# Performance work log

Hardware: AMD Instinct MI355X
Metric: run time of the kernel (lower is better)

## Reference

```python
import jax, jax.numpy as jnp
import numpy as np

B, N, H, D = 1024, 128, 128, 8  # batch, num_nodes (= num variables), hidden, diffusion size


def setup_inputs() -> dict:
    key = jax.random.key(0)
    ks = jax.random.split(key, 7)
    return {
        "x": jax.random.normal(ks[0], (B, N), dtype=jnp.float32),
        "f_weight": jax.random.normal(ks[1], (N, N, H), dtype=jnp.float32) * 0.1,
        "g_weight": jax.random.normal(ks[2], (N, N, H, D), dtype=jnp.float32) * 0.1,
        "Wf": jax.random.normal(ks[3], (N, H), dtype=jnp.float32) * (1.0 / np.sqrt(H)),
        "bf": jax.random.normal(ks[4], (N,), dtype=jnp.float32) * 0.01,
        "Wg": jax.random.normal(ks[5], (N, H), dtype=jnp.float32) * (1.0 / np.sqrt(H)),
        "bg": jax.random.normal(ks[6], (N,), dtype=jnp.float32) * 0.01,
    }


def reference(x, f_weight, g_weight, Wf, bf, Wg, bg):
    # Drift f: per node i, temp_i = x @ f_weight[i]  -> [B,H]; out_i = fc_i(elu(temp_i)) -> [B,1]
    # Batched over nodes as a single einsum instead of the original Python loop.
    temp_f = jnp.einsum('bn,inh->bih', x, f_weight)              # [B,N,H]
    f_out = jnp.einsum('bih,ih->bi', jax.nn.elu(temp_f), Wf) + bf  # [B,N]

    # Diffusion g: per node i, temp_i = x @ g_weight[i] -> [B,H,D]; fc_i applied over H per diffusion channel.
    temp_g = jnp.einsum('bn,inhd->bihd', x, g_weight)            # [B,N,H,D]
    g_out = jnp.einsum('bihd,ih->bid', jax.nn.elu(temp_g), Wg) + bg[None, :, None]  # [B,N,D]
    return f_out, g_out
```

## Files before the change

kernel.cpp:

```cpp
#include <hip/hip_runtime.h>
#include <hip/hip_bf16.h>


typedef unsigned short u16;
typedef __attribute__((ext_vector_type(8))) short bf16x8;
typedef __attribute__((ext_vector_type(4))) float f32x4;

typedef __attribute__((address_space(1))) const void* gas_ptr;
typedef __attribute__((address_space(3))) void* las_ptr;
#define GLOAD_LDS16(g, l) __builtin_amdgcn_global_load_lds((gas_ptr)(g), (las_ptr)(l), 16, 0, 0)

#define WS_W_ELEMS  ((size_t)128 * 1152 * 128)
#define WS_X_ELEMS  ((size_t)1024 * 128)
#define WS_NEED_BYTES ((WS_W_ELEMS + WS_X_ELEMS) * 2)

__device__ __forceinline__ u16 f2bf(float f) {
    unsigned int u = __float_as_uint(f);
    u += 0x7fffu + ((u >> 16) & 1u);
    return (u16)(u >> 16);
}
__device__ __forceinline__ uint32_t pack2bf(float a, float b) {
    return (uint32_t)f2bf(a) | ((uint32_t)f2bf(b) << 16);
}
__device__ __forceinline__ float elu(float v) {
    return v > 0.f ? v : __expf(v) - 1.f;
}

__global__ void sde_prepass_w(const float* __restrict__ fw, const float* __restrict__ gw,
                              u16* __restrict__ wsW) {
    __shared__ u16 tile[128 * 130];
    const int t   = threadIdx.x;
    const int blk = blockIdx.x;
    const int i   = blk / 9;
    const int ct  = blk % 9;
    const float* src;
    int sstride;
    if (ct < 8) { src = gw + (size_t)i * 131072 + ct * 128; sstride = 1024; }
    else        { src = fw + (size_t)i * 16384;             sstride = 128;  }
    const int c4 = (t & 31) * 4;
    const int np = (t >> 5) * 2;
    for (int p = 0; p < 8; ++p) {
        int n = p * 16 + np;
        float4 v0 = *(const float4*)&src[(size_t)n * sstride + c4];
        float4 v1 = *(const float4*)&src[(size_t)(n + 1) * sstride + c4];
        *(uint32_t*)&tile[(c4 + 0) * 130 + n] = pack2bf(v0.x, v1.x);
        *(uint32_t*)&tile[(c4 + 1) * 130 + n] = pack2bf(v0.y, v1.y);
        *(uint32_t*)&tile[(c4 + 2) * 130 + n] = pack2bf(v0.z, v1.z);
        *(uint32_t*)&tile[(c4 + 3) * 130 + n] = pack2bf(v0.w, v1.w);
    }
    __syncthreads();
    const int n0 = (t & 63) * 2;
    uint32_t* dst32 = (uint32_t*)wsW;
    for (int p = 0; p < 32; ++p) {
        int c = p * 4 + (t >> 6);
        uint32_t v = *(const uint32_t*)&tile[c * 130 + n0];
        dst32[((size_t)i * 1152 + ct * 128 + c) * 64 + (t & 63)] = v;
    }
}

__global__ void sde_prepass_x(const float* __restrict__ x, u16* __restrict__ wsX) {
    const int tid = blockIdx.x * 256 + threadIdx.x;
    float4 v = ((const float4*)x)[tid];
    ((uint2*)wsX)[tid] = make_uint2(pack2bf(v.x, v.y), pack2bf(v.z, v.w));
}

__global__ __launch_bounds__(256) void sde_mfma(
    const u16* __restrict__ wsAll,
    const float* __restrict__ Wf, const float* __restrict__ bfp,
    const float* __restrict__ Wg, const float* __restrict__ bgp,
    float* __restrict__ out)
{
    __shared__ u16 xs[128 * 128];
    __shared__ u16 wst[64 * 128];
    __shared__ float wgs[128];
    __shared__ float wfs[128];

    const int t    = threadIdx.x;
    const int bx   = blockIdx.x;
    const int i    = bx & 127;
    const int b0   = (bx >> 7) << 7;
    const int w    = t >> 6;
    const int lane = t & 63;
    const int l15  = lane & 15;
    const int quad = lane >> 4;
    const int rl   = lane >> 4;
    const int j16  = lane & 15;
    const int sw   = l15 & 7;

    const u16* wsW = wsAll;
    const u16* wsX = wsAll + WS_W_ELEMS;

    if (t < 128) { wgs[t] = Wg[i * 128 + t]; wfs[t] = Wf[i * 128 + t]; }

    {
        const char* srcX = (const char*)(wsX + (size_t)b0 * 128);
        #pragma unroll
        for (int r = 0; r < 8; ++r) {
            int row = w * 32 + r * 4 + rl;
            int soff = row * 256 + ((j16 ^ (row & 7)) << 4);
            GLOAD_LDS16(srcX + soff, (char*)xs + w * 8192 + r * 1024);
        }
    }

    float racc[8], frac[8];
    #pragma unroll
    for (int q = 0; q < 8; ++q) { racc[q] = 0.f; frac[q] = 0.f; }

    for (int ct = 0; ct < 18; ++ct) {
        {
            const char* srcW = (const char*)(wsW + ((size_t)i * 1152 + ct * 64) * 128);
            #pragma unroll
            for (int r = 0; r < 4; ++r) {
                int row = w * 16 + r * 4 + rl;
                int soff = row * 256 + ((j16 ^ (row & 7)) << 4);
                GLOAD_LDS16(srcW + soff, (char*)wst + w * 4096 + r * 1024);
            }
        }
        __syncthreads();

        f32x4 acc[2][4];
        #pragma unroll
        for (int rs = 0; rs < 2; ++rs)
            #pragma unroll
            for (int cs = 0; cs < 4; ++cs)
                acc[rs][cs] = (f32x4){0.f, 0.f, 0.f, 0.f};

        const int r0 = w * 32 + l15;
        #pragma unroll
        for (int kk = 0; kk < 4; ++kk) {
            const int co = ((kk * 4 + quad) ^ sw) << 3;
            bf16x8 a0 = *(const bf16x8*)&xs[r0 * 128 + co];
            bf16x8 a1 = *(const bf16x8*)&xs[(r0 + 16) * 128 + co];
            bf16x8 bv[4];
            #pragma unroll
            for (int cs = 0; cs < 4; ++cs)
                bv[cs] = *(const bf16x8*)&wst[(cs * 16 + l15) * 128 + co];
            #pragma unroll
            for (int cs = 0; cs < 4; ++cs) {
                acc[0][cs] = __builtin_amdgcn_mfma_f32_16x16x32_bf16(a0, bv[cs], acc[0][cs], 0, 0, 0);
                acc[1][cs] = __builtin_amdgcn_mfma_f32_16x16x32_bf16(a1, bv[cs], acc[1][cs], 0, 0, 0);
            }
        }

        if (ct < 16) {
            float wv[4];
            #pragma unroll
            for (int cs = 0; cs < 4; ++cs) wv[cs] = wgs[ct * 8 + cs * 2 + (l15 >> 3)];
            #pragma unroll
            for (int rs = 0; rs < 2; ++rs)
                #pragma unroll
                for (int rg = 0; rg < 4; ++rg) {
                    float p = elu(acc[rs][0][rg]) * wv[0] + elu(acc[rs][1][rg]) * wv[1]
                            + elu(acc[rs][2][rg]) * wv[2] + elu(acc[rs][3][rg]) * wv[3];
                    p += __shfl_xor(p, 8);
                    racc[rs * 4 + rg] += p;
                }
        } else {
            float wv[4];
            #pragma unroll
            for (int cs = 0; cs < 4; ++cs) wv[cs] = wfs[(ct - 16) * 64 + cs * 16 + l15];
            #pragma unroll
            for (int rs = 0; rs < 2; ++rs)
                #pragma unroll
                for (int rg = 0; rg < 4; ++rg) {
                    float p = elu(acc[rs][0][rg]) * wv[0] + elu(acc[rs][1][rg]) * wv[1]
                            + elu(acc[rs][2][rg]) * wv[2] + elu(acc[rs][3][rg]) * wv[3];
                    p += __shfl_xor(p, 1);
                    p += __shfl_xor(p, 2);
                    p += __shfl_xor(p, 4);
                    p += __shfl_xor(p, 8);
                    frac[rs * 4 + rg] += p;
                }
        }
        __syncthreads();
    }

    const float bfv = bfp[i], bgv = bgp[i];
    #pragma unroll
    for (int rs = 0; rs < 2; ++rs)
        #pragma unroll
        for (int rg = 0; rg < 4; ++rg) {
            int row = w * 32 + rs * 16 + quad * 4 + rg;
            size_t brow = (size_t)(b0 + row);
            if (l15 == 0)
                out[brow * 128 + i] = frac[rs * 4 + rg] + bfv;
            if (l15 < 8)
                out[(size_t)131072 + (brow * 128 + i) * 8 + (lane & 7)] = racc[rs * 4 + rg] + bgv;
        }
}

__global__ void sde_fallback(const float* __restrict__ x, const float* __restrict__ fw,
                             const float* __restrict__ gw,
                             const float* __restrict__ Wf, const float* __restrict__ bfp,
                             const float* __restrict__ Wg, const float* __restrict__ bgp,
                             float* __restrict__ out)
{
    __shared__ float xsh[64 * 128];
    const int t  = threadIdx.x;
    const int i  = blockIdx.x >> 4;
    const int b0 = (blockIdx.x & 15) << 6;
    for (int idx = t; idx < 64 * 128; idx += 64) xsh[idx] = x[(size_t)b0 * 128 + idx];
    __syncthreads();
    const float* xr  = &xsh[t * 128];
    const float* fwi = fw + (size_t)i * 16384;
    const float* gwi = gw + (size_t)i * 131072;
    float fa = 0.f;
    for (int h = 0; h < 128; ++h) {
        float tf = 0.f;
        for (int n = 0; n < 128; ++n) tf += xr[n] * fwi[n * 128 + h];
        fa += elu(tf) * Wf[i * 128 + h];
    }
    float ga[8];
    #pragma unroll
    for (int d = 0; d < 8; ++d) ga[d] = 0.f;
    for (int h = 0; h < 128; ++h) {
        float tg[8] = {0, 0, 0, 0, 0, 0, 0, 0};
        for (int n = 0; n < 128; ++n) {
            float xv = xr[n];
            const float* gp = gwi + ((size_t)n * 128 + h) * 8;
            #pragma unroll
            for (int d = 0; d < 8; ++d) tg[d] += xv * gp[d];
        }
        float wv = Wg[i * 128 + h];
        #pragma unroll
        for (int d = 0; d < 8; ++d) ga[d] += elu(tg[d]) * wv;
    }
    size_t b = (size_t)(b0 + t);
    out[b * 128 + i] = fa + bfp[i];
    #pragma unroll
    for (int d = 0; d < 8; ++d)
        out[(size_t)131072 + (b * 128 + i) * 8 + d] = ga[d] + bgp[i];
}

extern "C" void kernel_launch(void* const* d_in, const int* in_sizes, int n_in,
                              void* d_out, int out_size, void* d_ws, size_t ws_size,
                              hipStream_t stream) {
    const float* x  = (const float*)d_in[0];
    const float* fw = (const float*)d_in[1];
    const float* gw = (const float*)d_in[2];
    const float* Wf = (const float*)d_in[3];
    const float* bf = (const float*)d_in[4];
    const float* Wg = (const float*)d_in[5];
    const float* bg = (const float*)d_in[6];
    float* out = (float*)d_out;

    if (ws_size >= WS_NEED_BYTES) {
        u16* wsAll = (u16*)d_ws;
        sde_prepass_w<<<1152, 256, 0, stream>>>(fw, gw, wsAll);
        sde_prepass_x<<<128, 256, 0, stream>>>(x, wsAll + WS_W_ELEMS);
        sde_mfma<<<1024, 256, 0, stream>>>(wsAll, Wf, bf, Wg, bg, out);
    } else {
        sde_fallback<<<2048, 64, 0, stream>>>(x, fw, gw, Wf, bf, Wg, bg, out);
    }
}
```

Measured before the change: 185.0 us.

## Keep x fragments in registers, merge prepasses, defer cross-lane reductions

The MFMA kernel now loads its bf16 x A-fragments once from global memory into registers instead of staging a 32 KB x tile in LDS. This cuts LDS use per block and removes the repeated LDS reads of A inside the loop. The kernel adds launch_bounds(256,4) to favour higher occupancy, at the cost of more register pressure. The shuffle reductions that ran every tile are now done once per output at the end. The weight and x bf16 prepasses are merged into one kernel with a direct strided transpose that no longer uses an LDS tile.

```diff
diff --git a/kernel.cpp b/kernel.cpp
--- a/kernel.cpp
+++ b/kernel.cpp
@@ -4,6 +4,7 @@
 
 typedef unsigned short u16;
 typedef __attribute__((ext_vector_type(8))) short bf16x8;
+typedef __attribute__((ext_vector_type(8))) short short8;
 typedef __attribute__((ext_vector_type(4))) float f32x4;
 
 typedef __attribute__((address_space(1))) const void* gas_ptr;
@@ -26,51 +27,48 @@
     return v > 0.f ? v : __expf(v) - 1.f;
 }
 
-__global__ void sde_prepass_w(const float* __restrict__ fw, const float* __restrict__ gw,
-                              u16* __restrict__ wsW) {
-    __shared__ u16 tile[128 * 130];
-    const int t   = threadIdx.x;
-    const int blk = blockIdx.x;
-    const int i   = blk / 9;
-    const int ct  = blk % 9;
-    const float* src;
-    int sstride;
-    if (ct < 8) { src = gw + (size_t)i * 131072 + ct * 128; sstride = 1024; }
-    else        { src = fw + (size_t)i * 16384;             sstride = 128;  }
-    const int c4 = (t & 31) * 4;
-    const int np = (t >> 5) * 2;
-    for (int p = 0; p < 8; ++p) {
-        int n = p * 16 + np;
-        float4 v0 = *(const float4*)&src[(size_t)n * sstride + c4];
-        float4 v1 = *(const float4*)&src[(size_t)(n + 1) * sstride + c4];
-        *(uint32_t*)&tile[(c4 + 0) * 130 + n] = pack2bf(v0.x, v1.x);
-        *(uint32_t*)&tile[(c4 + 1) * 130 + n] = pack2bf(v0.y, v1.y);
-        *(uint32_t*)&tile[(c4 + 2) * 130 + n] = pack2bf(v0.z, v1.z);
-        *(uint32_t*)&tile[(c4 + 3) * 130 + n] = pack2bf(v0.w, v1.w);
-    }
-    __syncthreads();
-    const int n0 = (t & 63) * 2;
-    uint32_t* dst32 = (uint32_t*)wsW;
-    for (int p = 0; p < 32; ++p) {
-        int c = p * 4 + (t >> 6);
-        uint32_t v = *(const uint32_t*)&tile[c * 130 + n0];
-        dst32[((size_t)i * 1152 + ct * 128 + c) * 64 + (t & 63)] = v;
-    }
-}
-
-__global__ void sde_prepass_x(const float* __restrict__ x, u16* __restrict__ wsX) {
-    const int tid = blockIdx.x * 256 + threadIdx.x;
-    float4 v = ((const float4*)x)[tid];
-    ((uint2*)wsX)[tid] = make_uint2(pack2bf(v.x, v.y), pack2bf(v.z, v.w));
-}
-
-__global__ __launch_bounds__(256) void sde_mfma(
+__global__ void sde_prepass(const float* __restrict__ fw, const float* __restrict__ gw,
+                            const float* __restrict__ x, u16* __restrict__ wsW) {
+    const int bx = blockIdx.x;
+    const int t  = threadIdx.x;
+    if (bx < 8192) {
+        const int i  = bx >> 6;
+        const int c  = (((bx >> 4) & 3) << 8) + t;
+        const int n0 = (bx & 15) << 3;
+        const float* src = gw + (size_t)i * 131072;
+        float v[8];
+        #pragma unroll
+        for (int j = 0; j < 8; ++j) v[j] = src[(size_t)(n0 + j) * 1024 + c];
+        short8 o;
+        #pragma unroll
+        for (int j = 0; j < 8; ++j) o[j] = (short)f2bf(v[j]);
+        *(short8*)&wsW[((size_t)i * 1152 + c) * 128 + n0] = o;
+    } else if (bx < 9216) {
+        const int b2 = bx - 8192;
+        const int i  = b2 >> 3;
+        const int c  = t & 127;
+        const int n0 = (((b2 & 7) << 1) + (t >> 7)) << 3;
+        const float* src = fw + (size_t)i * 16384;
+        float v[8];
+        #pragma unroll
+        for (int j = 0; j < 8; ++j) v[j] = src[(size_t)(n0 + j) * 128 + c];
+        short8 o;
+        #pragma unroll
+        for (int j = 0; j < 8; ++j) o[j] = (short)f2bf(v[j]);
+        *(short8*)&wsW[((size_t)i * 1152 + 1024 + c) * 128 + n0] = o;
+    } else {
+        const int tid = (bx - 9216) * 256 + t;
+        float4 v = ((const float4*)x)[tid];
+        ((uint2*)(wsW + WS_W_ELEMS))[tid] = make_uint2(pack2bf(v.x, v.y), pack2bf(v.z, v.w));
+    }
+}
+
+__global__ __launch_bounds__(256, 4) void sde_mfma(
     const u16* __restrict__ wsAll,
     const float* __restrict__ Wf, const float* __restrict__ bfp,
     const float* __restrict__ Wg, const float* __restrict__ bgp,
     float* __restrict__ out)
 {
-    __shared__ u16 xs[128 * 128];
     __shared__ u16 wst[64 * 128];
     __shared__ float wgs[128];
     __shared__ float wfs[128];
@@ -92,13 +90,13 @@
 
     if (t < 128) { wgs[t] = Wg[i * 128 + t]; wfs[t] = Wf[i * 128 + t]; }
 
+    bf16x8 afrag[2][4];
     {
-        const char* srcX = (const char*)(wsX + (size_t)b0 * 128);
-        #pragma unroll
-        for (int r = 0; r < 8; ++r) {
-            int row = w * 32 + r * 4 + rl;
-            int soff = row * 256 + ((j16 ^ (row & 7)) << 4);
-            GLOAD_LDS16(srcX + soff, (char*)xs + w * 8192 + r * 1024);
+        const size_t r0 = (size_t)(b0 + w * 32 + l15) * 128 + quad * 8;
+        #pragma unroll
+        for (int kk = 0; kk < 4; ++kk) {
+            afrag[0][kk] = *(const bf16x8*)&wsX[r0 + kk * 32];
+            afrag[1][kk] = *(const bf16x8*)&wsX[r0 + 16 * 128 + kk * 32];
         }
     }
 
@@ -125,20 +123,17 @@
             for (int cs = 0; cs < 4; ++cs)
                 acc[rs][cs] = (f32x4){0.f, 0.f, 0.f, 0.f};
 
-        const int r0 = w * 32 + l15;
         #pragma unroll
         for (int kk = 0; kk < 4; ++kk) {
             const int co = ((kk * 4 + quad) ^ sw) << 3;
-            bf16x8 a0 = *(const bf16x8*)&xs[r0 * 128 + co];
-            bf16x8 a1 = *(const bf16x8*)&xs[(r0 + 16) * 128 + co];
             bf16x8 bv[4];
             #pragma unroll
             for (int cs = 0; cs < 4; ++cs)
                 bv[cs] = *(const bf16x8*)&wst[(cs * 16 + l15) * 128 + co];
             #pragma unroll
             for (int cs = 0; cs < 4; ++cs) {
-                acc[0][cs] = __builtin_amdgcn_mfma_f32_16x16x32_bf16(a0, bv[cs], acc[0][cs], 0, 0, 0);
-                acc[1][cs] = __builtin_amdgcn_mfma_f32_16x16x32_bf16(a1, bv[cs], acc[1][cs], 0, 0, 0);
+                acc[0][cs] = __builtin_amdgcn_mfma_f32_16x16x32_bf16(afrag[0][kk], bv[cs], acc[0][cs], 0, 0, 0);
+                acc[1][cs] = __builtin_amdgcn_mfma_f32_16x16x32_bf16(afrag[1][kk], bv[cs], acc[1][cs], 0, 0, 0);
             }
         }
 
@@ -150,10 +145,8 @@
             for (int rs = 0; rs < 2; ++rs)
                 #pragma unroll
                 for (int rg = 0; rg < 4; ++rg) {
-                    float p = elu(acc[rs][0][rg]) * wv[0] + elu(acc[rs][1][rg]) * wv[1]
-                            + elu(acc[rs][2][rg]) * wv[2] + elu(acc[rs][3][rg]) * wv[3];
-                    p += __shfl_xor(p, 8);
-                    racc[rs * 4 + rg] += p;
+                    racc[rs * 4 + rg] += elu(acc[rs][0][rg]) * wv[0] + elu(acc[rs][1][rg]) * wv[1]
+                                       + elu(acc[rs][2][rg]) * wv[2] + elu(acc[rs][3][rg]) * wv[3];
                 }
         } else {
             float wv[4];
@@ -163,13 +156,8 @@
             for (int rs = 0; rs < 2; ++rs)
                 #pragma unroll
                 for (int rg = 0; rg < 4; ++rg) {
-                    float p = elu(acc[rs][0][rg]) * wv[0] + elu(acc[rs][1][rg]) * wv[1]
-                            + elu(acc[rs][2][rg]) * wv[2] + elu(acc[rs][3][rg]) * wv[3];
-                    p += __shfl_xor(p, 1);
-                    p += __shfl_xor(p, 2);
-                    p += __shfl_xor(p, 4);
-                    p += __shfl_xor(p, 8);
-                    frac[rs * 4 + rg] += p;
+                    frac[rs * 4 + rg] += elu(acc[rs][0][rg]) * wv[0] + elu(acc[rs][1][rg]) * wv[1]
+                                       + elu(acc[rs][2][rg]) * wv[2] + elu(acc[rs][3][rg]) * wv[3];
                 }
         }
         __syncthreads();
@@ -180,12 +168,19 @@
     for (int rs = 0; rs < 2; ++rs)
         #pragma unroll
         for (int rg = 0; rg < 4; ++rg) {
+            int q = rs * 4 + rg;
+            racc[q] += __shfl_xor(racc[q], 8);
+            float fsum = frac[q];
+            fsum += __shfl_xor(fsum, 1);
+            fsum += __shfl_xor(fsum, 2);
+            fsum += __shfl_xor(fsum, 4);
+            fsum += __shfl_xor(fsum, 8);
             int row = w * 32 + rs * 16 + quad * 4 + rg;
             size_t brow = (size_t)(b0 + row);
             if (l15 == 0)
-                out[brow * 128 + i] = frac[rs * 4 + rg] + bfv;
+                out[brow * 128 + i] = fsum + bfv;
             if (l15 < 8)
-                out[(size_t)131072 + (brow * 128 + i) * 8 + (lane & 7)] = racc[rs * 4 + rg] + bgv;
+                out[(size_t)131072 + (brow * 128 + i) * 8 + (lane & 7)] = racc[q] + bgv;
         }
 }
 
@@ -246,8 +241,7 @@
 
     if (ws_size >= WS_NEED_BYTES) {
         u16* wsAll = (u16*)d_ws;
-        sde_prepass_w<<<1152, 256, 0, stream>>>(fw, gw, wsAll);
-        sde_prepass_x<<<128, 256, 0, stream>>>(x, wsAll + WS_W_ELEMS);
+        sde_prepass<<<9344, 256, 0, stream>>>(fw, gw, x, wsAll);
         sde_mfma<<<1024, 256, 0, stream>>>(wsAll, Wf, bf, Wg, bg, out);
     } else {
         sde_fallback<<<2048, 64, 0, stream>>>(x, fw, gw, Wf, bf, Wg, bg, out);
```

Result: slower. 193.1 us (+4.4%).
